# Kernel optimization log

Hardware: AMD Instinct MI355X
Metric: run time of the kernel (lower is better)

Reference implementation:

```python
import jax, jax.numpy as jnp
import numpy as np

B, IN, OUT = 512, 1024, 1024

def setup_inputs() -> dict:
    key = jax.random.key(0)
    kx, kw = jax.random.split(key)
    X = jax.random.normal(kx, (B, IN), dtype=jnp.float32)
    W = jax.random.normal(kw, (OUT, IN), dtype=jnp.float32) * 0.02  # init_std=0.02
    return {"X": X, "W": W}

def reference(X, W):
    # Tropical (max-plus) matmul: Y[b, j] = max_i (X[b, i] + W[j, i]).
    # leaky_factor=1 / is_random=False -> plain hard max in forward.
    # [B, 1, IN] + [1, OUT, IN] -> max over IN -> [B, OUT]
    return jnp.max(X[:, None, :] + W[None, :, :], axis=-1)
```

## Files before the change

### kernel.cpp

```cpp
#include <hip/hip_runtime.h>
#include <stdint.h>


#define M_DIM 512
#define N_DIM 1024
#define K_DIM 1024
#define CAP 128

__global__ __launch_bounds__(256)
void w_spread(const float* __restrict__ W, float* __restrict__ spread) {
    __shared__ float smx[256];
    __shared__ float smn[256];
    const int tid = threadIdx.x;
    const int j = blockIdx.x;
    float4 v = ((const float4*)W)[j * (K_DIM / 4) + tid];
    smx[tid] = fmaxf(fmaxf(v.x, v.y), fmaxf(v.z, v.w));
    smn[tid] = fminf(fminf(v.x, v.y), fminf(v.z, v.w));
    __syncthreads();
    for (int s = 128; s > 0; s >>= 1) {
        if (tid < s) {
            smx[tid] = fmaxf(smx[tid], smx[tid + s]);
            smn[tid] = fminf(smn[tid], smn[tid + s]);
        }
        __syncthreads();
    }
    if (tid == 0) spread[j] = smx[0] - smn[0];
}

__global__ __launch_bounds__(256)
void emit_pruned(const float* __restrict__ X, const float* __restrict__ W,
                 const float* __restrict__ spread, float* __restrict__ out) {
    __shared__ float red[256];
    __shared__ float sval[CAP];
    __shared__ int sidx[CAP];
    __shared__ int scnt;

    const int tid = threadIdx.x;
    const int b = blockIdx.x;

    {
        float4 sp = ((const float4*)spread)[tid];
        red[tid] = fmaxf(fmaxf(sp.x, sp.y), fmaxf(sp.z, sp.w));
    }
    if (tid == 0) scnt = 0;
    __syncthreads();
    for (int s = 128; s > 0; s >>= 1) {
        if (tid < s) red[tid] = fmaxf(red[tid], red[tid + s]);
        __syncthreads();
    }
    const float D = red[0] * 1.0001f + 1e-6f;
    __syncthreads();

    const float4 xv = ((const float4*)X)[b * (K_DIM / 4) + tid];
    red[tid] = fmaxf(fmaxf(xv.x, xv.y), fmaxf(xv.z, xv.w));
    __syncthreads();
    for (int s = 128; s > 0; s >>= 1) {
        if (tid < s) red[tid] = fmaxf(red[tid], red[tid + s]);
        __syncthreads();
    }
    const float thr = red[0] - D;

    const float xa[4] = {xv.x, xv.y, xv.z, xv.w};
#pragma unroll
    for (int c = 0; c < 4; c++) {
        if (xa[c] > thr) {
            int p = atomicAdd(&scnt, 1);
            if (p < CAP) { sidx[p] = tid * 4 + c; sval[p] = xa[c]; }
        }
    }
    __syncthreads();
    const int n = scnt;

    float4 acc = {-3.0e38f, -3.0e38f, -3.0e38f, -3.0e38f};
    float* accp = (float*)&acc;
    if (n <= CAP) {
        for (int c = 0; c < n; c++) {
            const int k = sidx[c];
            const float xk = sval[c];
            const float* wc = W + k;
#pragma unroll
            for (int q = 0; q < 4; q++) {
                const float w = wc[(size_t)(tid * 4 + q) * K_DIM];
                accp[q] = fmaxf(accp[q], xk + w);
            }
        }
    } else {
        for (int k = 0; k < K_DIM; k++) {
            const float xk = X[(size_t)b * K_DIM + k];
            const float* wc = W + k;
#pragma unroll
            for (int q = 0; q < 4; q++) {
                const float w = wc[(size_t)(tid * 4 + q) * K_DIM];
                accp[q] = fmaxf(accp[q], xk + w);
            }
        }
    }
    ((float4*)out)[b * (N_DIM / 4) + tid] = acc;
}

extern "C" void kernel_launch(void* const* d_in, const int* in_sizes, int n_in,
                              void* d_out, int out_size, void* d_ws, size_t ws_size,
                              hipStream_t stream) {
    const float* X = (const float*)d_in[0];
    const float* W = (const float*)d_in[1];
    float* out = (float*)d_out;
    float* spread = (float*)d_ws;

    w_spread<<<N_DIM, 256, 0, stream>>>(W, spread);
    emit_pruned<<<M_DIM, 256, 0, stream>>>(X, W, spread, out);
}
```

Baseline: 72.25 us.

## Transpose W into workspace for coalesced column reads and tiled spread

Replaces the per-row spread kernel with a tiled kernel that transposes W into workspace and emits per-tile row max/min partials. The main kernel reduces those partials to get the spread bound, then reads candidate rows of the transposed W as coalesced float4 loads instead of strided scalar column gathers. This targets the uncoalesced memory access in the pruned max-plus loop. In exchange, every call pays an extra full read and write of W for the transpose.

```diff
diff --git a/kernel.cpp b/kernel.cpp
--- a/kernel.cpp
+++ b/kernel.cpp
@@ -7,29 +7,72 @@
 #define K_DIM 1024
 #define CAP 128
 
+#define OFF_WT    0
+#define OFF_PMAX  (4u * 1024u * 1024u)
+#define OFF_PMIN  (OFF_PMAX + 64u * 1024u)
+
 __global__ __launch_bounds__(256)
-void w_spread(const float* __restrict__ W, float* __restrict__ spread) {
-    __shared__ float smx[256];
-    __shared__ float smn[256];
+void transpose_spread(const float* __restrict__ W, float* __restrict__ Wt,
+                      float* __restrict__ pmax, float* __restrict__ pmin) {
+    __shared__ float L[64][65];
+    __shared__ float smx[4][64];
+    __shared__ float smn[4][64];
+
     const int tid = threadIdx.x;
-    const int j = blockIdx.x;
-    float4 v = ((const float4*)W)[j * (K_DIM / 4) + tid];
-    smx[tid] = fmaxf(fmaxf(v.x, v.y), fmaxf(v.z, v.w));
-    smn[tid] = fminf(fminf(v.x, v.y), fminf(v.z, v.w));
+    const int kt = blockIdx.x;
+    const int jt = blockIdx.y;
+    const int k0 = kt * 64, j0 = jt * 64;
+
+    {
+        const int r = tid >> 2, q = tid & 3;
+        const float* g = &W[(size_t)(j0 + r) * K_DIM + k0 + q * 16];
+#pragma unroll
+        for (int t = 0; t < 4; t++) {
+            float4 f = *(const float4*)(g + 4 * t);
+            L[r][q * 16 + 4 * t + 0] = f.x;
+            L[r][q * 16 + 4 * t + 1] = f.y;
+            L[r][q * 16 + 4 * t + 2] = f.z;
+            L[r][q * 16 + 4 * t + 3] = f.w;
+        }
+    }
     __syncthreads();
-    for (int s = 128; s > 0; s >>= 1) {
-        if (tid < s) {
-            smx[tid] = fmaxf(smx[tid], smx[tid + s]);
-            smn[tid] = fminf(smn[tid], smn[tid + s]);
+
+    {
+        const int kk = tid >> 2, q = tid & 3;
+        float* o = &Wt[(size_t)(k0 + kk) * N_DIM + j0 + q * 16];
+#pragma unroll
+        for (int t = 0; t < 4; t++) {
+            float4 f = {L[q * 16 + 4 * t + 0][kk], L[q * 16 + 4 * t + 1][kk],
+                        L[q * 16 + 4 * t + 2][kk], L[q * 16 + 4 * t + 3][kk]};
+            *(float4*)(o + 4 * t) = f;
         }
-        __syncthreads();
     }
-    if (tid == 0) spread[j] = smx[0] - smn[0];
+
+    {
+        const int jl = tid & 63, seg = tid >> 6;
+        float mx = -3.0e38f, mn = 3.0e38f;
+#pragma unroll
+        for (int i = 0; i < 16; i++) {
+            float v = L[jl][seg * 16 + i];
+            mx = fmaxf(mx, v);
+            mn = fminf(mn, v);
+        }
+        smx[seg][jl] = mx;
+        smn[seg][jl] = mn;
+    }
+    __syncthreads();
+    if (tid < 64) {
+        float mx = fmaxf(fmaxf(smx[0][tid], smx[1][tid]), fmaxf(smx[2][tid], smx[3][tid]));
+        float mn = fminf(fminf(smn[0][tid], smn[1][tid]), fminf(smn[2][tid], smn[3][tid]));
+        pmax[kt * N_DIM + j0 + tid] = mx;
+        pmin[kt * N_DIM + j0 + tid] = mn;
+    }
 }
 
 __global__ __launch_bounds__(256)
-void emit_pruned(const float* __restrict__ X, const float* __restrict__ W,
-                 const float* __restrict__ spread, float* __restrict__ out) {
+void emit_pruned(const float* __restrict__ X, const float* __restrict__ Wt,
+                 const float* __restrict__ pmax, const float* __restrict__ pmin,
+                 float* __restrict__ out) {
     __shared__ float red[256];
     __shared__ float sval[CAP];
     __shared__ int sidx[CAP];
@@ -39,8 +82,20 @@
     const int b = blockIdx.x;
 
     {
-        float4 sp = ((const float4*)spread)[tid];
-        red[tid] = fmaxf(fmaxf(sp.x, sp.y), fmaxf(sp.z, sp.w));
+        float4 mx = {-3.0e38f, -3.0e38f, -3.0e38f, -3.0e38f};
+        float4 mn = {3.0e38f, 3.0e38f, 3.0e38f, 3.0e38f};
+#pragma unroll
+        for (int kt = 0; kt < 16; kt++) {
+            float4 a = ((const float4*)pmax)[kt * 256 + tid];
+            float4 i = ((const float4*)pmin)[kt * 256 + tid];
+            mx.x = fmaxf(mx.x, a.x); mx.y = fmaxf(mx.y, a.y);
+            mx.z = fmaxf(mx.z, a.z); mx.w = fmaxf(mx.w, a.w);
+            mn.x = fminf(mn.x, i.x); mn.y = fminf(mn.y, i.y);
+            mn.z = fminf(mn.z, i.z); mn.w = fminf(mn.w, i.w);
+        }
+        float s0 = fmaxf(mx.x - mn.x, mx.y - mn.y);
+        float s1 = fmaxf(mx.z - mn.z, mx.w - mn.w);
+        red[tid] = fmaxf(s0, s1);
     }
     if (tid == 0) scnt = 0;
     __syncthreads();
@@ -72,27 +127,24 @@
     const int n = scnt;
 
     float4 acc = {-3.0e38f, -3.0e38f, -3.0e38f, -3.0e38f};
-    float* accp = (float*)&acc;
     if (n <= CAP) {
         for (int c = 0; c < n; c++) {
             const int k = sidx[c];
             const float xk = sval[c];
-            const float* wc = W + k;
-#pragma unroll
-            for (int q = 0; q < 4; q++) {
-                const float w = wc[(size_t)(tid * 4 + q) * K_DIM];
-                accp[q] = fmaxf(accp[q], xk + w);
-            }
+            const float4 w = ((const float4*)Wt)[k * (N_DIM / 4) + tid];
+            acc.x = fmaxf(acc.x, xk + w.x);
+            acc.y = fmaxf(acc.y, xk + w.y);
+            acc.z = fmaxf(acc.z, xk + w.z);
+            acc.w = fmaxf(acc.w, xk + w.w);
         }
     } else {
         for (int k = 0; k < K_DIM; k++) {
             const float xk = X[(size_t)b * K_DIM + k];
-            const float* wc = W + k;
-#pragma unroll
-            for (int q = 0; q < 4; q++) {
-                const float w = wc[(size_t)(tid * 4 + q) * K_DIM];
-                accp[q] = fmaxf(accp[q], xk + w);
-            }
+            const float4 w = ((const float4*)Wt)[k * (N_DIM / 4) + tid];
+            acc.x = fmaxf(acc.x, xk + w.x);
+            acc.y = fmaxf(acc.y, xk + w.y);
+            acc.z = fmaxf(acc.z, xk + w.z);
+            acc.w = fmaxf(acc.w, xk + w.w);
         }
     }
     ((float4*)out)[b * (N_DIM / 4) + tid] = acc;
@@ -104,8 +156,12 @@
     const float* X = (const float*)d_in[0];
     const float* W = (const float*)d_in[1];
     float* out = (float*)d_out;
-    float* spread = (float*)d_ws;
 
-    w_spread<<<N_DIM, 256, 0, stream>>>(W, spread);
-    emit_pruned<<<M_DIM, 256, 0, stream>>>(X, W, spread, out);
+    char* ws = (char*)d_ws;
+    float* Wt   = (float*)(ws + OFF_WT);
+    float* pmax = (float*)(ws + OFF_PMAX);
+    float* pmin = (float*)(ws + OFF_PMIN);
+
+    transpose_spread<<<dim3(K_DIM / 64, N_DIM / 64), 256, 0, stream>>>(W, Wt, pmax, pmin);
+    emit_pruned<<<M_DIM, 256, 0, stream>>>(X, Wt, pmax, pmin, out);
 }
```

After: 66.69 us. -7.7%, faster.
